# Optimization experiments

Hardware: AMD Instinct MI355X
Metric: run time of the kernel (lower is better)

The kernel has to match this reference:

```python
import jax, jax.numpy as jnp
import numpy as np

B, T, N = 128, 64, 9
F_IN = 10
D_ENC = 128
HID = 256
H = 4
C = HID // H
EPS = 1e-5


def _build_edges(b, t):
    # chain adjacency + self loops (as in build_graph), then PyG GATv2Conv
    # remove_self_loops before re-adding mean-filled self loops at runtime.
    A = np.zeros((N, N), dtype=bool)
    i = np.arange(N - 1)
    A[i, i + 1] = True
    A[i + 1, i] = True
    A |= np.eye(N, dtype=bool)
    se = np.argwhere(A).T                       # [2, 25]
    e0 = se.shape[1]
    spatial = np.tile(se, (1, t)) + (np.repeat(np.arange(t), e0) * N)[None, :]
    s = np.arange(N * (t - 1))
    temporal = np.stack([s, s + N])             # forward-in-time edges
    single = np.concatenate([spatial, temporal], axis=1)
    eg = single.shape[1]
    ei = np.tile(single, (1, b)) + (np.repeat(np.arange(b), eg) * (t * N))[None, :]
    ei = ei[:, ei[0] != ei[1]]                  # remove_self_loops
    return jnp.asarray(ei[0]), jnp.asarray(ei[1])


def _forward(node_feats, enc_W, enc_b, layers):
    num_nodes = B * T * N
    types = np.array([0] * 7 + [1, 2])
    onehot = np.eye(3, dtype=np.float32)[types]
    dist = np.abs(np.arange(N) - 7).astype(np.float32)  # chain dist to eef (node 7)
    static = jnp.asarray(np.concatenate([onehot, dist[:, None]], axis=1))  # [N,4]
    feats = jnp.concatenate(
        [node_feats, jnp.broadcast_to(static, (B, T, N, 4))], axis=-1)
    # per-node-type encoders (all same dims -> batched einsum)
    x = (jnp.einsum('btnf,ndf->btnd', feats, enc_W) + enc_b).reshape(num_nodes, D_ENC)
    pos = node_feats[..., :3].reshape(num_nodes, 3)
    src, dst = _build_edges(B, T)
    eattr = pos[dst] - pos[src]
    loops = jnp.arange(num_nodes)
    fill = jnp.broadcast_to(eattr.mean(axis=0), (num_nodes, 3))  # fill_value='mean'
    src = jnp.concatenate([src, loops])
    dst = jnp.concatenate([dst, loops])
    eattr = jnp.concatenate([eattr, fill], axis=0)

    for (lW, lb, rW, rb, att, eW, sW, bias, g, b) in layers:
        xl = (x @ lW.T + lb).reshape(num_nodes, H, C)   # source transform
        xr = (x @ rW.T + rb).reshape(num_nodes, H, C)   # target transform
        em = (eattr @ eW.T).reshape(-1, H, C)
        m = jax.nn.leaky_relu(xl[src] + xr[dst] + em, 0.2)
        logit = jnp.einsum('ehc,hc->eh', m, att)        # [E,H]
        lmax = jax.ops.segment_max(logit, dst, num_segments=num_nodes)
        expv = jnp.exp(logit - lmax[dst])
        denom = jax.ops.segment_sum(expv, dst, num_segments=num_nodes)
        w = expv / denom[dst]                           # segment softmax over dst
        out = jax.ops.segment_sum(xl[src] * w[:, :, None], dst,
                                  num_segments=num_nodes)
        x = out.reshape(num_nodes, HID) + x @ sW.T + bias  # residual + bias
        mu = x.mean(-1, keepdims=True)
        var = ((x - mu) ** 2).mean(-1, keepdims=True)
        x = (x - mu) / jnp.sqrt(var + EPS) * g + b      # LayerNorm
        x = x * jax.nn.sigmoid(x)                       # SiLU
    return x.reshape(B, T * N, HID).mean(axis=1)        # global mean pool


def setup_inputs():
    key = jax.random.key(0)
    ks = iter(jax.random.split(key, 64))
    d = {"node_feats": jax.random.normal(next(ks), (B, T, N, F_IN), jnp.float32)}
    d["enc_W"] = jax.random.normal(next(ks), (N, D_ENC, F_IN + 4), jnp.float32) * 0.1
    d["enc_b"] = jnp.zeros((N, D_ENC), jnp.float32)
    dims = [D_ENC, HID, HID]
    for i in range(3):
        din = dims[i]
        d[f"l{i}_lW"] = jax.random.normal(next(ks), (HID, din), jnp.float32) * 0.05
        d[f"l{i}_lb"] = jnp.zeros((HID,), jnp.float32)
        d[f"l{i}_rW"] = jax.random.normal(next(ks), (HID, din), jnp.float32) * 0.05
        d[f"l{i}_rb"] = jnp.zeros((HID,), jnp.float32)
        d[f"l{i}_att"] = jax.random.normal(next(ks), (H, C), jnp.float32) * 0.1
        d[f"l{i}_eW"] = jax.random.normal(next(ks), (HID, 3), jnp.float32) * 0.1
        d[f"l{i}_sW"] = jax.random.normal(next(ks), (HID, din), jnp.float32) * 0.05
        d[f"l{i}_bias"] = jnp.zeros((HID,), jnp.float32)
        d[f"l{i}_g"] = jnp.ones((HID,), jnp.float32)
        d[f"l{i}_b"] = jnp.zeros((HID,), jnp.float32)
    return d


def reference(node_feats, enc_W, enc_b,
              l0_lW, l0_lb, l0_rW, l0_rb, l0_att, l0_eW, l0_sW, l0_bias, l0_g, l0_b,
              l1_lW, l1_lb, l1_rW, l1_rb, l1_att, l1_eW, l1_sW, l1_bias, l1_g, l1_b,
              l2_lW, l2_lb, l2_rW, l2_rb, l2_att, l2_eW, l2_sW, l2_bias, l2_g, l2_b):
    layers = [
        (l0_lW, l0_lb, l0_rW, l0_rb, l0_att, l0_eW, l0_sW, l0_bias, l0_g, l0_b),
        (l1_lW, l1_lb, l1_rW, l1_rb, l1_att, l1_eW, l1_sW, l1_bias, l1_g, l1_b),
        (l2_lW, l2_lb, l2_rW, l2_rb, l2_att, l2_eW, l2_sW, l2_bias, l2_g, l2_b),
    ]
    return _forward(node_feats, enc_W, enc_b, layers)
```

## Files before the change

kernel.cpp:

```cpp
#include <hip/hip_runtime.h>
#include <hip/hip_bf16.h>
#include <math.h>

#define NODES 73728
#define BB    128
#define TT    64
#define NN    9
#define LDX   256
#define E_REAL 203648.0f
#define NARR  33

typedef _Float16 half8 __attribute__((ext_vector_type(8)));
typedef _Float16 half4 __attribute__((ext_vector_type(4)));
typedef float f32x4 __attribute__((ext_vector_type(4)));

__device__ __forceinline__ float bfdec(unsigned short u) {
  return __uint_as_float(((unsigned)u) << 16);
}
__device__ __forceinline__ unsigned short f2h(float x) {
  _Float16 h = (_Float16)x;
  return __builtin_bit_cast(unsigned short, h);
}

#if __has_builtin(__builtin_amdgcn_fdot2)
#define DOT2(a, b, c) __builtin_amdgcn_fdot2((a), (b), (c), false)
#else
#define DOT2(a, b, c) ((c) + (float)(a)[0] * (float)(b)[0] + (float)(a)[1] * (float)(b)[1])
#endif
#define D2(v, k) __builtin_shufflevector((v), (v), 2 * (k), 2 * (k) + 1)

#define MFMA16(a, b, c) __builtin_amdgcn_mfma_f32_16x16x32_f16((a), (b), (c), 0, 0, 0)
#define SB0() __builtin_amdgcn_sched_barrier(0)

__device__ __forceinline__ void gl_lds16(const _Float16* g, _Float16* l) {
  __builtin_amdgcn_global_load_lds(
      (const __attribute__((address_space(1))) void*)g,
      (__attribute__((address_space(3))) void*)l, 16, 0, 0);
}

__global__ __launch_bounds__(256) void detect_kernel(const unsigned short* __restrict__ raw,
                                                     float* __restrict__ flag) {
  __shared__ float sm[256];
  float mx = 0.f;
  for (int i = threadIdx.x; i < 2048; i += 256) mx = fmaxf(mx, fabsf(bfdec(raw[2 * i])));
  sm[threadIdx.x] = mx;
  __syncthreads();
  for (int s = 128; s > 0; s >>= 1) {
    if (threadIdx.x < s) sm[threadIdx.x] = fmaxf(sm[threadIdx.x], sm[threadIdx.x + s]);
    __syncthreads();
  }
  if (threadIdx.x == 0) flag[0] = (sm[0] > 1000.f) ? 1.f : 0.f;
}

struct CvtArgs { const void* src[NARR]; int size[NARR]; int off[NARR]; };

__global__ __launch_bounds__(256) void convert_kernel(CvtArgs a, const float* __restrict__ flag,
                                                      float* __restrict__ dst,
                                                      _Float16* __restrict__ dsth) {
  int i = blockIdx.y;
  int sz = a.size[i];
  bool isf32 = flag[0] > 0.5f;
  const float* sf = (const float*)a.src[i];
  const unsigned short* sh = (const unsigned short*)a.src[i];
  float* d = dst + a.off[i];
  _Float16* dh = dsth + a.off[i];
  for (int j = blockIdx.x * 256 + threadIdx.x; j < sz; j += gridDim.x * 256) {
    float v = isf32 ? sf[j] : bfdec(sh[j]);
    d[j] = v;
    dh[j] = (_Float16)v;
  }
}

__global__ __launch_bounds__(256) void encoder_kernel(const float* __restrict__ nf,
    const float* __restrict__ encW, const float* __restrict__ encb, _Float16* __restrict__ Xh) {
  int tid = threadIdx.x;
  int v = blockIdx.x * 16 + (tid >> 4);
  int d0 = (tid & 15) << 3;
  int n = v % NN;
  float f[14];
#pragma unroll
  for (int i = 0; i < 10; i++) f[i] = nf[(size_t)v * 10 + i];
  f[10] = (n < 7) ? 1.f : 0.f;
  f[11] = (n == 7) ? 1.f : 0.f;
  f[12] = (n == 8) ? 1.f : 0.f;
  f[13] = fabsf((float)(n - 7));
  half8 o;
#pragma unroll
  for (int j = 0; j < 8; j++) {
    int d = d0 + j;
    const float* w = &encW[((size_t)n * 128 + d) * 14];
    float s = encb[n * 128 + d];
#pragma unroll
    for (int i = 0; i < 14; i++) s = fmaf(f[i], w[i], s);
    o[j] = (_Float16)s;
  }
  *(half8*)&Xh[(size_t)v * LDX + d0] = o;
}

__global__ __launch_bounds__(256) void fill_kernel(const float* __restrict__ nf,
                                                   float* __restrict__ fill) {
  __shared__ float sx[256], sy[256], sz[256];
  int tid = threadIdx.x;
  float ax = 0.f, ay = 0.f, az = 0.f;
  for (int p = tid; p < BB * NN; p += 256) {
    int b = p / NN, n = p - b * NN;
    size_t late  = (((size_t)b * TT + (TT - 1)) * NN + n) * 10;
    size_t early = (((size_t)b * TT) * NN + n) * 10;
    ax += nf[late + 0] - nf[early + 0];
    ay += nf[late + 1] - nf[early + 1];
    az += nf[late + 2] - nf[early + 2];
  }
  sx[tid] = ax; sy[tid] = ay; sz[tid] = az;
  __syncthreads();
  for (int s = 128; s > 0; s >>= 1) {
    if (tid < s) { sx[tid] += sx[tid + s]; sy[tid] += sy[tid + s]; sz[tid] += sz[tid + s]; }
    __syncthreads();
  }
  if (tid == 0) { fill[0] = sx[0] / E_REAL; fill[1] = sy[0] / E_REAL; fill[2] = sz[0] / E_REAL; }
}

template <int K>
__global__ __launch_bounds__(512, 4) void fused3_kernel(
    const _Float16* __restrict__ Xin, _Float16* __restrict__ Xout,
    const _Float16* __restrict__ lW, const float* __restrict__ lb,
    const _Float16* __restrict__ rW, const float* __restrict__ rb,
    const _Float16* __restrict__ sW, const float* __restrict__ sb,
    const float* __restrict__ nf, const float* __restrict__ fill,
    const _Float16* __restrict__ atth, const _Float16* __restrict__ ewh,
    const float* __restrict__ gamma, const float* __restrict__ beta,
    float* pool_out, int do_pool) {
  __shared__ union {
    _Float16 B[8 * 3072];
    struct {
      unsigned short xl[64][264];
      unsigned short epi[32][264];
    } s;
    float pacc[8][256];
  } sh;
  int tid = threadIdx.x;
  int row0 = blockIdx.x * 32;
  const int lane = tid & 63, wv = tid >> 6;
  const int quad = lane >> 4, mrow = lane & 15;
  const int bchunk = (lane & 3) ^ ((lane >> 3) & 3);
  const int rchunk = quad ^ ((mrow >> 1) & 3);
  _Float16* ring = sh.B + wv * 3072;
  const size_t wcol = (size_t)(wv * 32 + (lane >> 2));
  constexpr int NK = K >> 5;
  constexpr size_t wstep = (size_t)16 * K;
  const _Float16* lsrc  = lW + wcol * K + bchunk * 8;
  const _Float16* lsrc2 = lsrc + wstep;
  const _Float16* rsrc  = rW + wcol * K + bchunk * 8;
  const _Float16* rsrc2 = rsrc + wstep;
  const _Float16* ssrc  = sW + wcol * K + bchunk * 8;
  const _Float16* ssrc2 = ssrc + wstep;

  const _Float16* ap[4];
#pragma unroll
  for (int tl = 0; tl < 4; tl++) {
    int ar = row0 - 16 + tl * 16 + mrow;
    ar = ar < 0 ? 0 : (ar >= NODES ? NODES - 1 : ar);
    ap[tl] = Xin + (size_t)ar * LDX + quad * 8;
  }

  f32x4 accL[4][2] = {};
  f32x4 accR[2][2] = {};
  f32x4 accS[2][2] = {};
  half8 ab[2][4];

#pragma unroll
  for (int tl = 0; tl < 4; tl++) ab[0][tl] = *(const half8*)ap[tl];
  SB0();
  gl_lds16(lsrc, ring);        gl_lds16(lsrc2, ring + 512);
  gl_lds16(rsrc, ring + 1024); gl_lds16(rsrc2, ring + 1536);
  gl_lds16(ssrc, ring + 2048); gl_lds16(ssrc2, ring + 2560);
  SB0();

#pragma unroll
  for (int t = 0; t < NK; t++) {
    constexpr int _dummy = 0; (void)_dummy;
    const bool more = (t + 1 < NK);
    const int kn = (t + 1) << 5;
    if (more) {
#pragma unroll
      for (int tl = 0; tl < 4; tl++) ab[(t + 1) & 1][tl] = *(const half8*)(ap[tl] + kn);
    }
    SB0();
    if (more) asm volatile("s_waitcnt vmcnt(8)" ::: "memory");
    else      asm volatile("s_waitcnt vmcnt(4)" ::: "memory");
    SB0();
    {
      half8 b0 = *(const half8*)&ring[(0 * 16 + mrow) * 32 + rchunk * 8];
      half8 b1 = *(const half8*)&ring[(1 * 16 + mrow) * 32 + rchunk * 8];
#pragma unroll
      for (int tl = 0; tl < 4; tl++) {
        accL[tl][0] = MFMA16(ab[t & 1][tl], b0, accL[tl][0]);
        accL[tl][1] = MFMA16(ab[t & 1][tl], b1, accL[tl][1]);
      }
    }
    SB0();
    if (more) { gl_lds16(lsrc + kn, ring); gl_lds16(lsrc2 + kn, ring + 512); }
    SB0();
    if (more) asm volatile("s_waitcnt vmcnt(8)" ::: "memory");
    else      asm volatile("s_waitcnt vmcnt(2)" ::: "memory");
    SB0();
    {
      const _Float16* bb = ring + 1024;
      half8 b0 = *(const half8*)&bb[(0 * 16 + mrow) * 32 + rchunk * 8];
      half8 b1 = *(const half8*)&bb[(1 * 16 + mrow) * 32 + rchunk * 8];
      accR[0][0] = MFMA16(ab[t & 1][1], b0, accR[0][0]);
      accR[1][0] = MFMA16(ab[t & 1][2], b0, accR[1][0]);
      accR[0][1] = MFMA16(ab[t & 1][1], b1, accR[0][1]);
      accR[1][1] = MFMA16(ab[t & 1][2], b1, accR[1][1]);
    }
    SB0();
    if (more) { gl_lds16(rsrc + kn, ring + 1024); gl_lds16(rsrc2 + kn, ring + 1536); }
    SB0();
    if (more) asm volatile("s_waitcnt vmcnt(8)" ::: "memory");
    else      asm volatile("s_waitcnt vmcnt(0)" ::: "memory");
    SB0();
    {
      const _Float16* bb = ring + 2048;
      half8 b0 = *(const half8*)&bb[(0 * 16 + mrow) * 32 + rchunk * 8];
      half8 b1 = *(const half8*)&bb[(1 * 16 + mrow) * 32 + rchunk * 8];
      accS[0][0] = MFMA16(ab[t & 1][1], b0, accS[0][0]);
      accS[1][0] = MFMA16(ab[t & 1][2], b0, accS[1][0]);
      accS[0][1] = MFMA16(ab[t & 1][1], b1, accS[0][1]);
      accS[1][1] = MFMA16(ab[t & 1][2], b1, accS[1][1]);
    }
    SB0();
    if (more) { gl_lds16(ssrc + kn, ring + 2048); gl_lds16(ssrc2 + kn, ring + 2560); }
    SB0();
  }

  __syncthreads();

  {
    int quad_ = lane >> 4, mrow_ = lane & 15;
#pragma unroll
    for (int tl = 0; tl < 4; tl++)
#pragma unroll
      for (int ct = 0; ct < 2; ct++) {
        int col = wv * 32 + ct * 16 + mrow_;
        float bs = lb[col];
#pragma unroll
        for (int r = 0; r < 4; r++)
          sh.s.xl[tl * 16 + quad_ * 4 + r][col] = f2h(accL[tl][ct][r] + bs);
      }
#pragma unroll
    for (int rt = 0; rt < 2; rt++)
#pragma unroll
      for (int ct = 0; ct < 2; ct++) {
        int col = wv * 32 + ct * 16 + mrow_;
        float bs = rb[col];
#pragma unroll
        for (int r = 0; r < 4; r++)
          sh.s.epi[rt * 16 + quad_ * 4 + r][col] = f2h(accR[rt][ct][r] + bs);
      }
  }
  __syncthreads();

  {
    int g = lane >> 4;
    int l = lane & 15;
    int ch0 = l << 4;
    half8 att_lo = *(const half8*)&atth[ch0];
    half8 att_hi = *(const half8*)&atth[ch0 + 8];
    half8 ew0l, ew1l, ew2l, ew0h, ew1h, ew2h;
#pragma unroll
    for (int j = 0; j < 8; j++) {
      ew0l[j] = ewh[(ch0 + j) * 3 + 0];      ew0h[j] = ewh[(ch0 + 8 + j) * 3 + 0];
      ew1l[j] = ewh[(ch0 + j) * 3 + 1];      ew1h[j] = ewh[(ch0 + 8 + j) * 3 + 1];
      ew2l[j] = ewh[(ch0 + j) * 3 + 2];      ew2h[j] = ewh[(ch0 + 8 + j) * 3 + 2];
    }
    float f0 = fill[0], f1 = fill[1], f2 = fill[2];
    int r = wv * 4 + g;
    int v = row0 + r;
    int n = v % NN;
    int t = (v / NN) & 63;
    int srcs[4] = { v, (n > 0) ? v - 1 : v, (n < NN - 1) ? v + 1 : v, (t > 0) ? v - NN : v };
    bool valid[4] = { true, n > 0, n < NN - 1, t > 0 };
    float px = nf[(size_t)v * 10 + 0];
    float py = nf[(size_t)v * 10 + 1];
    float pz = nf[(size_t)v * 10 + 2];
    _Float16* erow = (_Float16*)sh.s.epi[r];
    half8 xr_lo = *(const half8*)&erow[ch0];
    half8 xr_hi = *(const half8*)&erow[ch0 + 8];
    half8 xls[4][2];
    float lg[4];
#pragma unroll
    for (int e = 0; e < 4; e++) {
      int s = srcs[e];
      float a0, a1, a2;
      if (e == 0) { a0 = f0; a1 = f1; a2 = f2; }
      else {
        a0 = px - nf[(size_t)s * 10 + 0];
        a1 = py - nf[(size_t)s * 10 + 1];
        a2 = pz - nf[(size_t)s * 10 + 2];
      }
      _Float16 h0 = (_Float16)a0, h1 = (_Float16)a1, h2 = (_Float16)a2;
      const _Float16* xrow = (const _Float16*)sh.s.xl[s - row0 + 16];
      xls[e][0] = *(const half8*)&xrow[ch0];
      xls[e][1] = *(const half8*)&xrow[ch0 + 8];
      half8 mlo = (xr_lo + xls[e][0]) + (ew0l * h0 + ew1l * h1 + ew2l * h2);
      half8 mhi = (xr_hi + xls[e][1]) + (ew0h * h0 + ew1h * h1 + ew2h * h2);
      mlo = __builtin_elementwise_max(mlo, mlo * (_Float16)0.2f);
      mhi = __builtin_elementwise_max(mhi, mhi * (_Float16)0.2f);
      float p = 0.f;
      p = DOT2(D2(mlo, 0), D2(att_lo, 0), p);
      p = DOT2(D2(mlo, 1), D2(att_lo, 1), p);
      p = DOT2(D2(mlo, 2), D2(att_lo, 2), p);
      p = DOT2(D2(mlo, 3), D2(att_lo, 3), p);
      p = DOT2(D2(mhi, 0), D2(att_hi, 0), p);
      p = DOT2(D2(mhi, 1), D2(att_hi, 1), p);
      p = DOT2(D2(mhi, 2), D2(att_hi, 2), p);
      p = DOT2(D2(mhi, 3), D2(att_hi, 3), p);
      p += __shfl_xor(p, 1);
      p += __shfl_xor(p, 2);
      lg[e] = valid[e] ? p : -1e30f;
    }
    float mx = fmaxf(fmaxf(lg[0], lg[1]), fmaxf(lg[2], lg[3]));
    float w0 = __expf(lg[0] - mx), w1 = __expf(lg[1] - mx);
    float w2 = __expf(lg[2] - mx), w3 = __expf(lg[3] - mx);
    float inv = 1.f / (w0 + w1 + w2 + w3);
    float wv4[4] = { w0, w1, w2, w3 };
    half8 agg_lo = { 0, 0, 0, 0, 0, 0, 0, 0 };
    half8 agg_hi = { 0, 0, 0, 0, 0, 0, 0, 0 };
#pragma unroll
    for (int e = 0; e < 4; e++) {
      _Float16 wh = (_Float16)(wv4[e] * inv);
      agg_lo = agg_lo + xls[e][0] * wh;
      agg_hi = agg_hi + xls[e][1] * wh;
    }
    *(half8*)&erow[ch0] = agg_lo;
    *(half8*)&erow[ch0 + 8] = agg_hi;
  }
  __syncthreads();

  {
    int quad_ = lane >> 4, mrow_ = lane & 15;
#pragma unroll
    for (int rt = 0; rt < 2; rt++)
#pragma unroll
      for (int ct = 0; ct < 2; ct++) {
        int col = wv * 32 + ct * 16 + mrow_;
        float bs = sb[col];
#pragma unroll
        for (int rr = 0; rr < 4; rr++) {
          int row = rt * 16 + quad_ * 4 + rr;
          _Float16 ag = *(const _Float16*)&sh.s.epi[row][col];
          sh.s.epi[row][col] = f2h(accS[rt][ct][rr] + bs + (float)ag);
        }
      }
  }
  __syncthreads();

  {
    int cc = lane << 2;
    float gm[4], bt[4];
#pragma unroll
    for (int i = 0; i < 4; i++) { gm[i] = gamma[cc + i]; bt[i] = beta[cc + i]; }
    float psum[4] = { 0.f, 0.f, 0.f, 0.f };
    for (int k = 0; k < 4; k++) {
      int r = wv * 4 + k;
      int v = row0 + r;
      const _Float16* erow = (const _Float16*)sh.s.epi[r];
      half4 x4 = *(const half4*)&erow[cc];
      float xv[4] = { (float)x4[0], (float)x4[1], (float)x4[2], (float)x4[3] };
      float s1 = xv[0] + xv[1] + xv[2] + xv[3];
#pragma unroll
      for (int off = 1; off < 64; off <<= 1) s1 += __shfl_xor(s1, off);
      float mu = s1 * (1.f / 256.f);
      float s2 = 0.f;
#pragma unroll
      for (int i = 0; i < 4; i++) { float d = xv[i] - mu; s2 = fmaf(d, d, s2); }
#pragma unroll
      for (int off = 1; off < 64; off <<= 1) s2 += __shfl_xor(s2, off);
      float rs = rsqrtf(s2 * (1.f / 256.f) + 1e-5f);
      half4 o;
#pragma unroll
      for (int i = 0; i < 4; i++) {
        float y = (xv[i] - mu) * rs * gm[i] + bt[i];
        float z = y * (1.f / (1.f + __expf(-y)));
        o[i] = (_Float16)z;
        psum[i] += z;
      }
      *(half4*)&Xout[(size_t)v * LDX + cc] = o;
    }
    if (do_pool) {
      __syncthreads();
#pragma unroll
      for (int i = 0; i < 4; i++) sh.pacc[wv][cc + i] = psum[i];
      __syncthreads();
      if (wv == 0) {
        int b = row0 / 576;
#pragma unroll
        for (int i = 0; i < 4; i++) {
          float s = 0.f;
#pragma unroll
          for (int w = 0; w < 8; w++) s += sh.pacc[w][cc + i];
          atomicAdd(&pool_out[b * 256 + cc + i], s * (1.f / 576.f));
        }
      }
    }
  }
}

extern "C" void kernel_launch(void* const* d_in, const int* in_sizes, int n_in,
                              void* d_out, int out_size, void* d_ws, size_t ws_size,
                              hipStream_t stream) {
  static const int kSize[NARR] = {
    737280, 16128, 1152,
    32768, 256, 32768, 256, 256, 768, 32768, 256, 256, 256,
    65536, 256, 65536, 256, 256, 768, 65536, 256, 256, 256,
    65536, 256, 65536, 256, 256, 768, 65536, 256, 256, 256
  };
  if (n_in != NARR || out_size != BB * 256) return;
  for (int i = 0; i < NARR; i++) if (in_sizes[i] != kSize[i]) return;

  CvtArgs ca;
  int off = 0;
  for (int i = 0; i < NARR; i++) { ca.src[i] = d_in[i]; ca.size[i] = kSize[i]; ca.off[i] = off; off += kSize[i]; }
  const int PRM_ELEMS = off;

  const size_t OFF_FLAG = 0;
  const size_t OFF_FILL = 16;
  const size_t OFF_PRM  = 256;
  const size_t OFF_PRMH = OFF_PRM + (size_t)PRM_ELEMS * 4;
  const size_t OFF_X0   = OFF_PRMH + (size_t)PRM_ELEMS * 2;
  const size_t OFF_X1   = OFF_X0 + (size_t)NODES * LDX * 2;
  const size_t NEED     = OFF_X1 + (size_t)NODES * LDX * 2;
  if (ws_size < NEED) return;

  char* ws = (char*)d_ws;
  float*     flag = (float*)(ws + OFF_FLAG);
  float*     fill = (float*)(ws + OFF_FILL);
  float*     prm  = (float*)(ws + OFF_PRM);
  _Float16*  prmh = (_Float16*)(ws + OFF_PRMH);
  _Float16*  X0   = (_Float16*)(ws + OFF_X0);
  _Float16*  X1   = (_Float16*)(ws + OFF_X1);

  hipMemsetAsync(d_out, 0, (size_t)out_size * 4, stream);
  detect_kernel<<<1, 256, 0, stream>>>((const unsigned short*)d_in[0], flag);
  convert_kernel<<<dim3(128, NARR), 256, 0, stream>>>(ca, flag, prm, prmh);

  const float* nf   = prm + ca.off[0];
  const float* encW = prm + ca.off[1];
  const float* encb = prm + ca.off[2];

  encoder_kernel<<<NODES / 16, 256, 0, stream>>>(nf, encW, encb, X0);
  fill_kernel<<<1, 256, 0, stream>>>(nf, fill);

  _Float16* Xa = X0;
  _Float16* Xb = X1;
  for (int L = 0; L < 3; L++) {
    const _Float16* lWh = prmh + ca.off[3 + L * 10 + 0];
    const float*    lb  = prm  + ca.off[3 + L * 10 + 1];
    const _Float16* rWh = prmh + ca.off[3 + L * 10 + 2];
    const float*    rb  = prm  + ca.off[3 + L * 10 + 3];
    const _Float16* atth= prmh + ca.off[3 + L * 10 + 4];
    const _Float16* ewhp= prmh + ca.off[3 + L * 10 + 5];
    const _Float16* sWh = prmh + ca.off[3 + L * 10 + 6];
    const float*    sb  = prm  + ca.off[3 + L * 10 + 7];
    const float*    g   = prm  + ca.off[3 + L * 10 + 8];
    const float*    b   = prm  + ca.off[3 + L * 10 + 9];
    if (L == 0)
      fused3_kernel<128><<<NODES / 32, 512, 0, stream>>>(Xa, Xb, lWh, lb, rWh, rb, sWh, sb,
                                                         nf, fill, atth, ewhp, g, b,
                                                         (float*)d_out, 0);
    else
      fused3_kernel<256><<<NODES / 32, 512, 0, stream>>>(Xa, Xb, lWh, lb, rWh, rb, sWh, sb,
                                                         nf, fill, atth, ewhp, g, b,
                                                         (float*)d_out, (L == 2) ? 1 : 0);
    _Float16* tmp = Xa; Xa = Xb; Xb = tmp;
  }
}
```

Before: 502.7 us.

## Shrink xl halo to 48 rows, swizzle block order, raise MFMA priority

The source-transform tile drops from 64 to 48 rows, with a 12-row halo instead of 16, so each block does 3 instead of 4 MFMA row tiles for lW. The owned 32 rows are loaded separately into their own fragments for the R and S products. Block IDs are swizzled across 8 groups, and s_setprio is raised around the MFMA sections to favour math issue. This cuts lW MFMA work by a quarter but adds two extra global A-fragment loads per k-step and changes the vmcnt accounting.

```diff
diff --git a/kernel.cpp b/kernel.cpp
--- a/kernel.cpp
+++ b/kernel.cpp
@@ -132,13 +132,15 @@
   __shared__ union {
     _Float16 B[8 * 3072];
     struct {
-      unsigned short xl[64][264];
+      unsigned short xl[48][264];
       unsigned short epi[32][264];
     } s;
     float pacc[8][256];
   } sh;
   int tid = threadIdx.x;
-  int row0 = blockIdx.x * 32;
+  int bid = blockIdx.x;
+  int swz = (bid & 7) * ((int)gridDim.x >> 3) + (bid >> 3);
+  int row0 = swz * 32;
   const int lane = tid & 63, wv = tid >> 6;
   const int quad = lane >> 4, mrow = lane & 15;
   const int bchunk = (lane & 3) ^ ((lane >> 3) & 3);
@@ -154,21 +156,26 @@
   const _Float16* ssrc  = sW + wcol * K + bchunk * 8;
   const _Float16* ssrc2 = ssrc + wstep;
 
-  const _Float16* ap[4];
-#pragma unroll
-  for (int tl = 0; tl < 4; tl++) {
-    int ar = row0 - 16 + tl * 16 + mrow;
+  const _Float16* ap[3];
+#pragma unroll
+  for (int tl = 0; tl < 3; tl++) {
+    int ar = row0 - 12 + tl * 16 + mrow;
     ar = ar < 0 ? 0 : (ar >= NODES ? NODES - 1 : ar);
     ap[tl] = Xin + (size_t)ar * LDX + quad * 8;
   }
-
-  f32x4 accL[4][2] = {};
+  const _Float16* aro0 = Xin + (size_t)(row0 + mrow) * LDX + quad * 8;
+  const _Float16* aro1 = Xin + (size_t)(row0 + 16 + mrow) * LDX + quad * 8;
+
+  f32x4 accL[3][2] = {};
   f32x4 accR[2][2] = {};
   f32x4 accS[2][2] = {};
-  half8 ab[2][4];
-
-#pragma unroll
-  for (int tl = 0; tl < 4; tl++) ab[0][tl] = *(const half8*)ap[tl];
+  half8 ab[2][3];
+  half8 ob[2][2];
+
+#pragma unroll
+  for (int tl = 0; tl < 3; tl++) ab[0][tl] = *(const half8*)ap[tl];
+  ob[0][0] = *(const half8*)aro0;
+  ob[0][1] = *(const half8*)aro1;
   SB0();
   gl_lds16(lsrc, ring);        gl_lds16(lsrc2, ring + 512);
   gl_lds16(rsrc, ring + 1024); gl_lds16(rsrc2, ring + 1536);
@@ -177,56 +184,63 @@
 
 #pragma unroll
   for (int t = 0; t < NK; t++) {
-    constexpr int _dummy = 0; (void)_dummy;
     const bool more = (t + 1 < NK);
     const int kn = (t + 1) << 5;
     if (more) {
 #pragma unroll
-      for (int tl = 0; tl < 4; tl++) ab[(t + 1) & 1][tl] = *(const half8*)(ap[tl] + kn);
-    }
-    SB0();
-    if (more) asm volatile("s_waitcnt vmcnt(8)" ::: "memory");
+      for (int tl = 0; tl < 3; tl++) ab[(t + 1) & 1][tl] = *(const half8*)(ap[tl] + kn);
+      ob[(t + 1) & 1][0] = *(const half8*)(aro0 + kn);
+      ob[(t + 1) & 1][1] = *(const half8*)(aro1 + kn);
+    }
+    SB0();
+    if (more) asm volatile("s_waitcnt vmcnt(9)" ::: "memory");
     else      asm volatile("s_waitcnt vmcnt(4)" ::: "memory");
     SB0();
+    __builtin_amdgcn_s_setprio(1);
     {
       half8 b0 = *(const half8*)&ring[(0 * 16 + mrow) * 32 + rchunk * 8];
       half8 b1 = *(const half8*)&ring[(1 * 16 + mrow) * 32 + rchunk * 8];
 #pragma unroll
-      for (int tl = 0; tl < 4; tl++) {
+      for (int tl = 0; tl < 3; tl++) {
         accL[tl][0] = MFMA16(ab[t & 1][tl], b0, accL[tl][0]);
         accL[tl][1] = MFMA16(ab[t & 1][tl], b1, accL[tl][1]);
       }
     }
+    __builtin_amdgcn_s_setprio(0);
     SB0();
     if (more) { gl_lds16(lsrc + kn, ring); gl_lds16(lsrc2 + kn, ring + 512); }
     SB0();
-    if (more) asm volatile("s_waitcnt vmcnt(8)" ::: "memory");
+    if (more) asm volatile("s_waitcnt vmcnt(9)" ::: "memory");
     else      asm volatile("s_waitcnt vmcnt(2)" ::: "memory");
     SB0();
+    __builtin_amdgcn_s_setprio(1);
     {
       const _Float16* bb = ring + 1024;
       half8 b0 = *(const half8*)&bb[(0 * 16 + mrow) * 32 + rchunk * 8];
       half8 b1 = *(const half8*)&bb[(1 * 16 + mrow) * 32 + rchunk * 8];
-      accR[0][0] = MFMA16(ab[t & 1][1], b0, accR[0][0]);
-      accR[1][0] = MFMA16(ab[t & 1][2], b0, accR[1][0]);
-      accR[0][1] = MFMA16(ab[t & 1][1], b1, accR[0][1]);
-      accR[1][1] = MFMA16(ab[t & 1][2], b1, accR[1][1]);
-    }
+      accR[0][0] = MFMA16(ob[t & 1][0], b0, accR[0][0]);
+      accR[1][0] = MFMA16(ob[t & 1][1], b0, accR[1][0]);
+      accR[0][1] = MFMA16(ob[t & 1][0], b1, accR[0][1]);
+      accR[1][1] = MFMA16(ob[t & 1][1], b1, accR[1][1]);
+    }
+    __builtin_amdgcn_s_setprio(0);
     SB0();
     if (more) { gl_lds16(rsrc + kn, ring + 1024); gl_lds16(rsrc2 + kn, ring + 1536); }
     SB0();
-    if (more) asm volatile("s_waitcnt vmcnt(8)" ::: "memory");
+    if (more) asm volatile("s_waitcnt vmcnt(9)" ::: "memory");
     else      asm volatile("s_waitcnt vmcnt(0)" ::: "memory");
     SB0();
+    __builtin_amdgcn_s_setprio(1);
     {
       const _Float16* bb = ring + 2048;
       half8 b0 = *(const half8*)&bb[(0 * 16 + mrow) * 32 + rchunk * 8];
       half8 b1 = *(const half8*)&bb[(1 * 16 + mrow) * 32 + rchunk * 8];
-      accS[0][0] = MFMA16(ab[t & 1][1], b0, accS[0][0]);
-      accS[1][0] = MFMA16(ab[t & 1][2], b0, accS[1][0]);
-      accS[0][1] = MFMA16(ab[t & 1][1], b1, accS[0][1]);
-      accS[1][1] = MFMA16(ab[t & 1][2], b1, accS[1][1]);
-    }
+      accS[0][0] = MFMA16(ob[t & 1][0], b0, accS[0][0]);
+      accS[1][0] = MFMA16(ob[t & 1][1], b0, accS[1][0]);
+      accS[0][1] = MFMA16(ob[t & 1][0], b1, accS[0][1]);
+      accS[1][1] = MFMA16(ob[t & 1][1], b1, accS[1][1]);
+    }
+    __builtin_amdgcn_s_setprio(0);
     SB0();
     if (more) { gl_lds16(ssrc + kn, ring + 2048); gl_lds16(ssrc2 + kn, ring + 2560); }
     SB0();
@@ -237,7 +251,7 @@
   {
     int quad_ = lane >> 4, mrow_ = lane & 15;
 #pragma unroll
-    for (int tl = 0; tl < 4; tl++)
+    for (int tl = 0; tl < 3; tl++)
 #pragma unroll
       for (int ct = 0; ct < 2; ct++) {
         int col = wv * 32 + ct * 16 + mrow_;
@@ -298,7 +312,7 @@
         a2 = pz - nf[(size_t)s * 10 + 2];
       }
       _Float16 h0 = (_Float16)a0, h1 = (_Float16)a1, h2 = (_Float16)a2;
-      const _Float16* xrow = (const _Float16*)sh.s.xl[s - row0 + 16];
+      const _Float16* xrow = (const _Float16*)sh.s.xl[s - row0 + 12];
       xls[e][0] = *(const half8*)&xrow[ch0];
       xls[e][1] = *(const half8*)&xrow[ch0 + 8];
       half8 mlo = (xr_lo + xls[e][0]) + (ew0l * h0 + ew1l * h1 + ew2l * h2);
```

Result: slower. 545.4 us (+8.5%).
